# Kernel tuning notes

Measured on AMD Instinct MI355X. Metric: run time of the kernel, lower is better.

## Reference

```python
import jax, jax.numpy as jnp
import numpy as np

N = 100000
E = 1600000
F_IN = 64
H = 128
D_OUT = 1
G = 512  # number of graphs
EPS = 1e-5


def setup_inputs() -> dict:
    key = jax.random.key(0)
    ks = jax.random.split(key, 16)
    x = jax.random.normal(ks[0], (N, F_IN), dtype=jnp.float32)
    edge_index = jax.random.randint(ks[1], (2, E), 0, N, dtype=jnp.int64)
    batch = jnp.sort(jax.random.randint(ks[2], (N,), 0, G, dtype=jnp.int64))
    def lin(k, fin, fout):
        s = 1.0 / np.sqrt(fin)
        k1, k2 = jax.random.split(k)
        return (jax.random.uniform(k1, (fin, fout), jnp.float32, -s, s),
                jax.random.uniform(k2, (fout,), jnp.float32, -s, s))
    fc1_w, fc1_b = lin(ks[3], F_IN, H)
    gc1_w, gc1_b = lin(ks[4], H, H)
    gc2_w, gc2_b = lin(ks[5], H, H)
    fc2_w, fc2_b = lin(ks[6], H, D_OUT)
    gn1_g = jnp.ones((H,), jnp.float32); gn1_b = jnp.zeros((H,), jnp.float32)
    gn2_g = jnp.ones((H,), jnp.float32); gn2_b = jnp.zeros((H,), jnp.float32)
    return dict(x=x, edge_index=edge_index, batch=batch,
                fc1_w=fc1_w, fc1_b=fc1_b, gc1_w=gc1_w, gc1_b=gc1_b,
                gn1_g=gn1_g, gn1_b=gn1_b, gc2_w=gc2_w, gc2_b=gc2_b,
                gn2_g=gn2_g, gn2_b=gn2_b, fc2_w=fc2_w, fc2_b=fc2_b)


def gcn_conv(x, src, dst, deg_inv_sqrt, w, b):
    # x: [N,H]; symmetric-normalized aggregation with self-loops already in src/dst
    h = x @ w  # [N, H_out]
    norm = deg_inv_sqrt[src] * deg_inv_sqrt[dst]  # [E+N]
    msgs = h[src] * norm[:, None]
    out = jax.ops.segment_sum(msgs, dst, num_segments=N)
    return out + b


def graph_layernorm(x, batch, gamma, beta, counts):
    # PyG LayerNorm mode='graph': normalize over all nodes+channels per graph
    denom = jnp.maximum(counts * x.shape[1], 1.0)  # [G]
    mean = jax.ops.segment_sum(x.sum(-1), batch, num_segments=G) / denom
    xc = x - mean[batch][:, None]
    var = jax.ops.segment_sum((xc * xc).sum(-1), batch, num_segments=G) / denom
    inv = jax.lax.rsqrt(var + EPS)
    return xc * inv[batch][:, None] * gamma + beta


def reference(x, edge_index, batch, fc1_w, fc1_b, gc1_w, gc1_b, gn1_g, gn1_b,
              gc2_w, gc2_b, gn2_g, gn2_b, fc2_w, fc2_b):
    loops = jnp.arange(N, dtype=edge_index.dtype)
    src = jnp.concatenate([edge_index[0], loops])
    dst = jnp.concatenate([edge_index[1], loops])
    deg = jax.ops.segment_sum(jnp.ones_like(dst, dtype=x.dtype), dst, num_segments=N)
    deg_inv_sqrt = jnp.where(deg > 0, jax.lax.rsqrt(jnp.maximum(deg, 1.0)), 0.0)
    counts = jax.ops.segment_sum(jnp.ones_like(batch, dtype=x.dtype), batch, num_segments=G)

    hx = x @ fc1_w + fc1_b
    h = jax.nn.relu(graph_layernorm(gcn_conv(hx, src, dst, deg_inv_sqrt, gc1_w, gc1_b), batch, gn1_g, gn1_b, counts))
    h = jax.nn.relu(graph_layernorm(gcn_conv(h, src, dst, deg_inv_sqrt, gc2_w, gc2_b), batch, gn2_g, gn2_b, counts))
    pooled = jax.ops.segment_sum(h, batch, num_segments=G) / jnp.maximum(counts, 1.0)[:, None]
    return pooled @ fc2_w + fc2_b  # [G, D_OUT]
```

## Files before the change

### kernel.cpp

```cpp
#include <hip/hip_runtime.h>

#define NN 100000
#define EE 1600000
#define FIN 64
#define HH 128
#define GG 512
#define EPSV 1e-5f

__global__ void initk(int* deg, int* cursor, int* counts,
                      float* gsum1, float* gsq1, float* gsum2, float* gsq2,
                      float* pooled) {
  int i = blockIdx.x * 256 + threadIdx.x;
  if (i < NN) { deg[i] = 1; cursor[i] = 0; }
  if (i < GG) { counts[i] = 0; gsum1[i] = 0.f; gsq1[i] = 0.f; gsum2[i] = 0.f; gsq2[i] = 0.f; }
  if (i < GG * HH) pooled[i] = 0.f;
}

__global__ void countk(const int* __restrict__ ei, const int* __restrict__ batch,
                       int* deg, int* counts) {
  int i = blockIdx.x * 256 + threadIdx.x;
  if (i < EE) atomicAdd(&deg[ei[EE + i]], 1);
  if (i < NN) atomicAdd(&counts[batch[i]], 1);
}

__global__ void disk(const int* __restrict__ deg, float* __restrict__ dis) {
  int i = blockIdx.x * 256 + threadIdx.x;
  if (i < NN) dis[i] = rsqrtf((float)deg[i]);
}

#define SCHUNK 1024
__global__ void scan1(const int* __restrict__ deg, int* __restrict__ bsum) {
  __shared__ int red[256];
  int b = blockIdx.x, t = threadIdx.x;
  int base = b * SCHUNK + t * 4;
  int s = 0;
#pragma unroll
  for (int i = 0; i < 4; i++) { int idx = base + i; if (idx < NN) s += deg[idx] - 1; }
  red[t] = s; __syncthreads();
  for (int o = 128; o > 0; o >>= 1) { if (t < o) red[t] += red[t + o]; __syncthreads(); }
  if (t == 0) bsum[b] = red[0];
}

__global__ void scan2(const int* __restrict__ bsum, int* __restrict__ boff,
                      int* __restrict__ rowptr, int nblk) {
  if (threadIdx.x == 0 && blockIdx.x == 0) {
    int run = 0;
    for (int i = 0; i < nblk; i++) { boff[i] = run; run += bsum[i]; }
    rowptr[NN] = run;
  }
}

__global__ void scan3(const int* __restrict__ deg, const int* __restrict__ boff,
                      int* __restrict__ rowptr) {
  __shared__ int sc[2][256];
  int b = blockIdx.x, t = threadIdx.x;
  int base = b * SCHUNK + t * 4;
  int v[4]; int s = 0;
#pragma unroll
  for (int i = 0; i < 4; i++) {
    int idx = base + i;
    v[i] = (idx < NN) ? (deg[idx] - 1) : 0;
    s += v[i];
  }
  int pp = 0;
  sc[0][t] = s; __syncthreads();
  for (int o = 1; o < 256; o <<= 1) {
    int val = sc[pp][t];
    if (t >= o) val += sc[pp][t - o];
    sc[pp ^ 1][t] = val; __syncthreads();
    pp ^= 1;
  }
  int excl = sc[pp][t] - s;
  int p = boff[b] + excl;
#pragma unroll
  for (int i = 0; i < 4; i++) {
    int idx = base + i;
    if (idx < NN) rowptr[idx] = p;
    p += v[i];
  }
}

__global__ void scatterk(const int* __restrict__ ei, int* cursor,
                         const int* __restrict__ rowptr, int* __restrict__ colsrc) {
  int e = blockIdx.x * 256 + threadIdx.x;
  if (e >= EE) return;
  int d = ei[EE + e];
  int pos = rowptr[d] + atomicAdd(&cursor[d], 1);
  colsrc[pos] = ei[e];
}

__global__ void prepw(const float* __restrict__ fc1w, const float* __restrict__ fc1b,
                      const float* __restrict__ gc1w,
                      float* __restrict__ Wp, float* __restrict__ c1) {
  int k = blockIdx.x, t = threadIdx.x;
  if (k < 64) {
    float s = 0.f;
    for (int j = 0; j < 128; j++) s = fmaf(fc1w[k * 128 + j], gc1w[j * 128 + t], s);
    Wp[k * 128 + t] = s;
  } else {
    float s = 0.f;
    for (int j = 0; j < 128; j++) s = fmaf(fc1b[j], gc1w[j * 128 + t], s);
    c1[t] = s;
  }
}

__global__ __launch_bounds__(256, 8)
void aggx(const float* __restrict__ X, const int* __restrict__ colsrc,
          const int* __restrict__ rowptr, const float* __restrict__ dis,
          float* __restrict__ Y, float* __restrict__ rowsum) {
  int wid = threadIdx.x >> 6;
  int n = blockIdx.x * 4 + wid;
  int lane = threadIdx.x & 63;
  int slot = lane >> 4, q = lane & 15;
  float di = dis[n];
  int rp0 = rowptr[n];
  int m = rowptr[n + 1] - rp0 + 1;
  float4 acc = make_float4(0.f, 0.f, 0.f, 0.f);
  float wsum = 0.f;
  int s[4];
#pragma unroll
  for (int j = 0; j < 4; j++) {
    int idx = 4 * j + slot;
    s[j] = (idx >= m - 1) ? n : colsrc[rp0 + idx];
  }
  int p = 0;
  for (; p + 15 < m; p += 16) {
    int sn[4];
#pragma unroll
    for (int j = 0; j < 4; j++) {
      int idx = p + 16 + 4 * j + slot;
      sn[j] = (idx >= m - 1) ? n : colsrc[rp0 + idx];
    }
    float w[4]; float4 h[4];
#pragma unroll
    for (int j = 0; j < 4; j++) {
      w[j] = dis[s[j]] * di;
      h[j] = *reinterpret_cast<const float4*>(&X[(size_t)s[j] * FIN + q * 4]);
    }
#pragma unroll
    for (int j = 0; j < 4; j++) {
      acc.x = fmaf(h[j].x, w[j], acc.x);
      acc.y = fmaf(h[j].y, w[j], acc.y);
      acc.z = fmaf(h[j].z, w[j], acc.z);
      acc.w = fmaf(h[j].w, w[j], acc.w);
      wsum += w[j];
    }
#pragma unroll
    for (int j = 0; j < 4; j++) s[j] = sn[j];
  }
  for (; p < m; p += 4) {
    int idx = p + slot;
    if (idx < m) {
      int sv = (idx == m - 1) ? n : colsrc[rp0 + idx];
      float w = dis[sv] * di;
      float4 h = *reinterpret_cast<const float4*>(&X[(size_t)sv * FIN + q * 4]);
      acc.x = fmaf(h.x, w, acc.x);
      acc.y = fmaf(h.y, w, acc.y);
      acc.z = fmaf(h.z, w, acc.z);
      acc.w = fmaf(h.w, w, acc.w);
      wsum += w;
    }
  }
  acc.x += __shfl_xor(acc.x, 16); acc.y += __shfl_xor(acc.y, 16);
  acc.z += __shfl_xor(acc.z, 16); acc.w += __shfl_xor(acc.w, 16);
  wsum  += __shfl_xor(wsum, 16);
  acc.x += __shfl_xor(acc.x, 32); acc.y += __shfl_xor(acc.y, 32);
  acc.z += __shfl_xor(acc.z, 32); acc.w += __shfl_xor(acc.w, 32);
  wsum  += __shfl_xor(wsum, 32);
  if (slot == 0) {
    *reinterpret_cast<float4*>(&Y[(size_t)n * FIN + q * 4]) = acc;
  }
  if (lane == 0) rowsum[n] = wsum;
}

__global__ void gemmA(const float* __restrict__ Y, const float* __restrict__ Wp,
                      const float* __restrict__ c1, const float* __restrict__ gc1b,
                      const float* __restrict__ rowsum, const int* __restrict__ batch,
                      float* __restrict__ A, float* __restrict__ gsum, float* __restrict__ gsq) {
  __shared__ float ys[8 * 64];
  __shared__ float l1[8][2], l2[8][2];
  int n0 = blockIdx.x * 8, t = threadIdx.x;
  reinterpret_cast<float4*>(ys)[t] =
      reinterpret_cast<const float4*>(Y + (size_t)n0 * 64)[t];
  __syncthreads();
  float cv = c1[t], bv = gc1b[t];
  float acc[8];
#pragma unroll
  for (int n = 0; n < 8; n++) acc[n] = bv;
#pragma unroll 4
  for (int k = 0; k < 64; k++) {
    float wv = Wp[k * 128 + t];
#pragma unroll
    for (int n = 0; n < 8; n++) acc[n] = fmaf(ys[n * 64 + k], wv, acc[n]);
  }
#pragma unroll
  for (int n = 0; n < 8; n++) {
    acc[n] = fmaf(rowsum[n0 + n], cv, acc[n]);
    A[(size_t)(n0 + n) * 128 + t] = acc[n];
  }
  int wid = t >> 6, lane = t & 63;
#pragma unroll
  for (int n = 0; n < 8; n++) {
    float s1v = acc[n], s2v = acc[n] * acc[n];
    for (int o = 32; o > 0; o >>= 1) {
      s1v += __shfl_down(s1v, o);
      s2v += __shfl_down(s2v, o);
    }
    if (lane == 0) { l1[n][wid] = s1v; l2[n][wid] = s2v; }
  }
  __syncthreads();
  if (t < 8) {
    int b = batch[n0 + t];
    atomicAdd(&gsum[b], l1[t][0] + l1[t][1]);
    atomicAdd(&gsq[b], l2[t][0] + l2[t][1]);
  }
}

template <bool LN>
__global__ void gemm128(const float* __restrict__ X, const float* __restrict__ W,
                        float* __restrict__ Y,
                        const int* __restrict__ batch,
                        const float* __restrict__ mean, const float* __restrict__ inv,
                        const float* __restrict__ gamma, const float* __restrict__ beta) {
  __shared__ float xs[8 * 128];
  int n0 = blockIdx.x * 8, t = threadIdx.x;
  const float* xb = X + (size_t)n0 * 128;
  if (LN) {
#pragma unroll
    for (int j = 0; j < 8; j++) {
      int node = n0 + j;
      int bb = batch[node];
      float v = xb[j * 128 + t];
      v = (v - mean[bb]) * inv[bb] * gamma[t] + beta[t];
      xs[j * 128 + t] = fmaxf(v, 0.f);
    }
  } else {
    for (int i = t; i < 1024; i += 128) xs[i] = xb[i];
  }
  __syncthreads();
  float acc[8];
#pragma unroll
  for (int n = 0; n < 8; n++) acc[n] = 0.f;
#pragma unroll 4
  for (int k = 0; k < 128; k++) {
    float wv = W[k * 128 + t];
#pragma unroll
    for (int n = 0; n < 8; n++) acc[n] = fmaf(xs[n * 128 + k], wv, acc[n]);
  }
#pragma unroll
  for (int n = 0; n < 8; n++) Y[(size_t)(n0 + n) * 128 + t] = acc[n];
}

__global__ __launch_bounds__(256, 8)
void aggk(const float* __restrict__ Hin, const int* __restrict__ colsrc,
          const int* __restrict__ rowptr, const float* __restrict__ dis,
          const float* __restrict__ bias, const int* __restrict__ batch,
          float* __restrict__ Yout, float* __restrict__ gsum, float* __restrict__ gsq) {
  int wid = threadIdx.x >> 6;
  int n = blockIdx.x * 4 + wid;
  int lane = threadIdx.x & 63;
  int half = lane >> 5, q = lane & 31;
  float di = dis[n];
  int rp0 = rowptr[n];
  int m = rowptr[n + 1] - rp0 + 1;
  float4 acc = make_float4(0.f, 0.f, 0.f, 0.f);
  int s[4];
#pragma unroll
  for (int j = 0; j < 4; j++) {
    int idx = 2 * j + half;
    s[j] = (idx >= m - 1) ? n : colsrc[rp0 + idx];
  }
  int p = 0;
  for (; p + 7 < m; p += 8) {
    int sn[4];
#pragma unroll
    for (int j = 0; j < 4; j++) {
      int idx = p + 8 + 2 * j + half;
      sn[j] = (idx >= m - 1) ? n : colsrc[rp0 + idx];
    }
    float w[4]; float4 h[4];
#pragma unroll
    for (int j = 0; j < 4; j++) {
      w[j] = dis[s[j]] * di;
      h[j] = *reinterpret_cast<const float4*>(&Hin[(size_t)s[j] * HH + q * 4]);
    }
#pragma unroll
    for (int j = 0; j < 4; j++) {
      acc.x = fmaf(h[j].x, w[j], acc.x);
      acc.y = fmaf(h[j].y, w[j], acc.y);
      acc.z = fmaf(h[j].z, w[j], acc.z);
      acc.w = fmaf(h[j].w, w[j], acc.w);
    }
#pragma unroll
    for (int j = 0; j < 4; j++) s[j] = sn[j];
  }
  for (; p < m; p += 2) {
    int idx = p + half;
    if (idx < m) {
      int sv = (idx == m - 1) ? n : colsrc[rp0 + idx];
      float w = dis[sv] * di;
      float4 h = *reinterpret_cast<const float4*>(&Hin[(size_t)sv * HH + q * 4]);
      acc.x = fmaf(h.x, w, acc.x);
      acc.y = fmaf(h.y, w, acc.y);
      acc.z = fmaf(h.z, w, acc.z);
      acc.w = fmaf(h.w, w, acc.w);
    }
  }
  acc.x += __shfl_xor(acc.x, 32);
  acc.y += __shfl_xor(acc.y, 32);
  acc.z += __shfl_xor(acc.z, 32);
  acc.w += __shfl_xor(acc.w, 32);
  float4 bv = *reinterpret_cast<const float4*>(&bias[q * 4]);
  acc.x += bv.x; acc.y += bv.y; acc.z += bv.z; acc.w += bv.w;
  if (half == 0) {
    *reinterpret_cast<float4*>(&Yout[(size_t)n * HH + q * 4]) = acc;
  }
  float s1 = acc.x + acc.y + acc.z + acc.w;
  float s2 = acc.x * acc.x + acc.y * acc.y + acc.z * acc.z + acc.w * acc.w;
  for (int o = 16; o > 0; o >>= 1) {
    s1 += __shfl_down(s1, o);
    s2 += __shfl_down(s2, o);
  }
  if (lane == 0) {
    int b = batch[n];
    atomicAdd(&gsum[b], s1);
    atomicAdd(&gsq[b], s2);
  }
}

__global__ void lnfinal(const float* __restrict__ gsum, const float* __restrict__ gsq,
                        const int* __restrict__ counts,
                        float* __restrict__ mean, float* __restrict__ inv) {
  int g = blockIdx.x * 256 + threadIdx.x;
  if (g >= GG) return;
  float denom = fmaxf((float)counts[g] * (float)HH, 1.f);
  float m = gsum[g] / denom;
  float v = gsq[g] / denom - m * m;
  mean[g] = m;
  inv[g] = rsqrtf(fmaxf(v, 0.f) + EPSV);
}

__global__ void poolk(const float* __restrict__ A, const int* __restrict__ batch,
                      const float* __restrict__ mean, const float* __restrict__ inv,
                      const float* __restrict__ gamma, const float* __restrict__ beta,
                      float* __restrict__ pooled) {
  int idx = blockIdx.x * 256 + threadIdx.x;
  if (idx >= NN * HH) return;
  int n = idx >> 7, ch = idx & 127;
  int b = batch[n];
  float v = (A[idx] - mean[b]) * inv[b] * gamma[ch] + beta[ch];
  v = fmaxf(v, 0.f);
  atomicAdd(&pooled[b * 128 + ch], v);
}

__global__ void finalk(const float* __restrict__ pooled, const int* __restrict__ counts,
                       const float* __restrict__ w, const float* __restrict__ b,
                       float* __restrict__ out) {
  int g = blockIdx.x, t = threadIdx.x;
  float cnt = fmaxf((float)counts[g], 1.f);
  float v = pooled[g * 128 + t] / cnt * w[t];
  for (int o = 32; o > 0; o >>= 1) v += __shfl_down(v, o);
  __shared__ float l[2];
  if ((t & 63) == 0) l[t >> 6] = v;
  __syncthreads();
  if (t == 0) out[g] = l[0] + l[1] + b[0];
}

extern "C" void kernel_launch(void* const* d_in, const int* in_sizes, int n_in,
                              void* d_out, int out_size, void* d_ws, size_t ws_size,
                              hipStream_t stream) {
  const float* x = (const float*)d_in[0];
  const int* ei = (const int*)d_in[1];
  const int* batch = (const int*)d_in[2];
  const float* fc1_w = (const float*)d_in[3];
  const float* fc1_b = (const float*)d_in[4];
  const float* gc1_w = (const float*)d_in[5];
  const float* gc1_b = (const float*)d_in[6];
  const float* gn1_g = (const float*)d_in[7];
  const float* gn1_b = (const float*)d_in[8];
  const float* gc2_w = (const float*)d_in[9];
  const float* gc2_b = (const float*)d_in[10];
  const float* gn2_g = (const float*)d_in[11];
  const float* gn2_b = (const float*)d_in[12];
  const float* fc2_w = (const float*)d_in[13];
  const float* fc2_b = (const float*)d_in[14];
  float* out = (float*)d_out;

  char* p = (char*)d_ws;
  auto alloc = [&](size_t bytes) { void* r = (void*)p; p += ((bytes + 255) / 256) * 256; return r; };
  float* A = (float*)alloc((size_t)NN * HH * 4);
  float* B = (float*)alloc((size_t)NN * HH * 4);
  float* Yx = B;
  int* colsrc = (int*)alloc((size_t)EE * 4);
  int* rowptr = (int*)alloc((size_t)(NN + 1) * 4);
  int* deg = (int*)alloc((size_t)NN * 4);
  int* cursor = (int*)alloc((size_t)NN * 4);
  float* dis = (float*)alloc((size_t)NN * 4);
  float* rowsum = (float*)alloc((size_t)NN * 4);
  int* counts = (int*)alloc((size_t)GG * 4);
  float* gsum1 = (float*)alloc((size_t)GG * 4);
  float* gsq1 = (float*)alloc((size_t)GG * 4);
  float* gsum2 = (float*)alloc((size_t)GG * 4);
  float* gsq2 = (float*)alloc((size_t)GG * 4);
  float* mean1 = (float*)alloc((size_t)GG * 4);
  float* inv1 = (float*)alloc((size_t)GG * 4);
  float* mean2 = (float*)alloc((size_t)GG * 4);
  float* inv2 = (float*)alloc((size_t)GG * 4);
  float* pooled = (float*)alloc((size_t)GG * HH * 4);
  float* Wp = (float*)alloc((size_t)64 * 128 * 4);
  float* c1 = (float*)alloc((size_t)128 * 4);
  int* bsum = (int*)alloc(1024);
  int* boff = (int*)alloc(1024);

  int nblk = (NN + SCHUNK - 1) / SCHUNK;

  initk<<<(NN + 255) / 256, 256, 0, stream>>>(deg, cursor, counts, gsum1, gsq1, gsum2, gsq2, pooled);
  countk<<<(EE + 255) / 256, 256, 0, stream>>>(ei, batch, deg, counts);
  disk<<<(NN + 255) / 256, 256, 0, stream>>>(deg, dis);
  scan1<<<nblk, 256, 0, stream>>>(deg, bsum);
  scan2<<<1, 64, 0, stream>>>(bsum, boff, rowptr, nblk);
  scan3<<<nblk, 256, 0, stream>>>(deg, boff, rowptr);
  scatterk<<<(EE + 255) / 256, 256, 0, stream>>>(ei, cursor, rowptr, colsrc);
  prepw<<<65, 128, 0, stream>>>(fc1_w, fc1_b, gc1_w, Wp, c1);

  aggx<<<NN / 4, 256, 0, stream>>>(x, colsrc, rowptr, dis, Yx, rowsum);
  gemmA<<<NN / 8, 128, 0, stream>>>(Yx, Wp, c1, gc1_b, rowsum, batch, A, gsum1, gsq1);
  lnfinal<<<(GG + 255) / 256, 256, 0, stream>>>(gsum1, gsq1, counts, mean1, inv1);
  gemm128<true><<<NN / 8, 128, 0, stream>>>(A, gc2_w, B, batch, mean1, inv1, gn1_g, gn1_b);
  aggk<<<NN / 4, 256, 0, stream>>>(B, colsrc, rowptr, dis, gc2_b, batch, A, gsum2, gsq2);
  lnfinal<<<(GG + 255) / 256, 256, 0, stream>>>(gsum2, gsq2, counts, mean2, inv2);
  poolk<<<(NN * HH + 255) / 256, 256, 0, stream>>>(A, batch, mean2, inv2, gn2_g, gn2_b, pooled);
  finalk<<<GG, 128, 0, stream>>>(pooled, counts, fc2_w, fc2_b, out);
}
```

Measured before the change: 1.040 ms.

## Store gathered node features in bf16 for both aggregation passes

Converts the input features x to bf16 in a new pre-pass and makes the second-layer GEMM write its output as bf16. Both gather-based aggregation kernels now read bf16 rows, so each gathered row moves half the bytes, and they accumulate in fp32. The per-lane layout is reworked so each lane handles 8 channels, which changes edge parallelism and the shuffle reductions. This adds an extra conversion kernel and lowers the precision of the aggregated features, which could affect accuracy tolerances.

```diff
diff --git a/kernel.cpp b/kernel.cpp
--- a/kernel.cpp
+++ b/kernel.cpp
@@ -6,6 +6,12 @@
 #define HH 128
 #define GG 512
 #define EPSV 1e-5f
+
+__device__ __forceinline__ unsigned short f2bf(float f) {
+  unsigned int u = __float_as_uint(f);
+  u = (u + 0x7FFFu + ((u >> 16) & 1u)) >> 16;
+  return (unsigned short)u;
+}
 
 __global__ void initk(int* deg, int* cursor, int* counts,
                       float* gsum1, float* gsq1, float* gsum2, float* gsq2,
@@ -14,6 +20,15 @@
   if (i < NN) { deg[i] = 1; cursor[i] = 0; }
   if (i < GG) { counts[i] = 0; gsum1[i] = 0.f; gsq1[i] = 0.f; gsum2[i] = 0.f; gsq2[i] = 0.f; }
   if (i < GG * HH) pooled[i] = 0.f;
+}
+
+__global__ void convx(const float* __restrict__ x, unsigned short* __restrict__ xb) {
+  int i = blockIdx.x * 256 + threadIdx.x;
+  if (i >= NN * FIN / 4) return;
+  float4 v = reinterpret_cast<const float4*>(x)[i];
+  ushort4 o;
+  o.x = f2bf(v.x); o.y = f2bf(v.y); o.z = f2bf(v.z); o.w = f2bf(v.w);
+  reinterpret_cast<ushort4*>(xb)[i] = o;
 }
 
 __global__ void countk(const int* __restrict__ ei, const int* __restrict__ batch,
@@ -105,70 +120,76 @@
 }
 
 __global__ __launch_bounds__(256, 8)
-void aggx(const float* __restrict__ X, const int* __restrict__ colsrc,
+void aggx(const unsigned short* __restrict__ X, const int* __restrict__ colsrc,
           const int* __restrict__ rowptr, const float* __restrict__ dis,
           float* __restrict__ Y, float* __restrict__ rowsum) {
   int wid = threadIdx.x >> 6;
   int n = blockIdx.x * 4 + wid;
   int lane = threadIdx.x & 63;
-  int slot = lane >> 4, q = lane & 15;
+  int slot = lane >> 3, q = lane & 7;
   float di = dis[n];
   int rp0 = rowptr[n];
   int m = rowptr[n + 1] - rp0 + 1;
-  float4 acc = make_float4(0.f, 0.f, 0.f, 0.f);
+  float acc[8];
+#pragma unroll
+  for (int k = 0; k < 8; k++) acc[k] = 0.f;
   float wsum = 0.f;
-  int s[4];
-#pragma unroll
-  for (int j = 0; j < 4; j++) {
-    int idx = 4 * j + slot;
-    s[j] = (idx >= m - 1) ? n : colsrc[rp0 + idx];
-  }
   int p = 0;
   for (; p + 15 < m; p += 16) {
-    int sn[4];
-#pragma unroll
-    for (int j = 0; j < 4; j++) {
-      int idx = p + 16 + 4 * j + slot;
-      sn[j] = (idx >= m - 1) ? n : colsrc[rp0 + idx];
-    }
-    float w[4]; float4 h[4];
-#pragma unroll
-    for (int j = 0; j < 4; j++) {
+    int s[2]; float w[2]; uint4 h[2];
+#pragma unroll
+    for (int j = 0; j < 2; j++) {
+      int idx = p + 8 * j + slot;
+      s[j] = (idx == m - 1) ? n : colsrc[rp0 + idx];
+    }
+#pragma unroll
+    for (int j = 0; j < 2; j++) {
       w[j] = dis[s[j]] * di;
-      h[j] = *reinterpret_cast<const float4*>(&X[(size_t)s[j] * FIN + q * 4]);
-    }
-#pragma unroll
-    for (int j = 0; j < 4; j++) {
-      acc.x = fmaf(h[j].x, w[j], acc.x);
-      acc.y = fmaf(h[j].y, w[j], acc.y);
-      acc.z = fmaf(h[j].z, w[j], acc.z);
-      acc.w = fmaf(h[j].w, w[j], acc.w);
+      h[j] = reinterpret_cast<const uint4*>(X + (size_t)s[j] * FIN)[q];
+    }
+#pragma unroll
+    for (int j = 0; j < 2; j++) {
+      unsigned int u;
+      u = h[j].x; acc[0] = fmaf(__uint_as_float(u << 16), w[j], acc[0]);
+                  acc[1] = fmaf(__uint_as_float(u & 0xFFFF0000u), w[j], acc[1]);
+      u = h[j].y; acc[2] = fmaf(__uint_as_float(u << 16), w[j], acc[2]);
+                  acc[3] = fmaf(__uint_as_float(u & 0xFFFF0000u), w[j], acc[3]);
+      u = h[j].z; acc[4] = fmaf(__uint_as_float(u << 16), w[j], acc[4]);
+                  acc[5] = fmaf(__uint_as_float(u & 0xFFFF0000u), w[j], acc[5]);
+      u = h[j].w; acc[6] = fmaf(__uint_as_float(u << 16), w[j], acc[6]);
+                  acc[7] = fmaf(__uint_as_float(u & 0xFFFF0000u), w[j], acc[7]);
       wsum += w[j];
     }
-#pragma unroll
-    for (int j = 0; j < 4; j++) s[j] = sn[j];
-  }
-  for (; p < m; p += 4) {
+  }
+  for (; p < m; p += 8) {
     int idx = p + slot;
     if (idx < m) {
       int sv = (idx == m - 1) ? n : colsrc[rp0 + idx];
       float w = dis[sv] * di;
-      float4 h = *reinterpret_cast<const float4*>(&X[(size_t)sv * FIN + q * 4]);
-      acc.x = fmaf(h.x, w, acc.x);
-      acc.y = fmaf(h.y, w, acc.y);
-      acc.z = fmaf(h.z, w, acc.z);
-      acc.w = fmaf(h.w, w, acc.w);
+      uint4 h = reinterpret_cast<const uint4*>(X + (size_t)sv * FIN)[q];
+      unsigned int u;
+      u = h.x; acc[0] = fmaf(__uint_as_float(u << 16), w, acc[0]);
+               acc[1] = fmaf(__uint_as_float(u & 0xFFFF0000u), w, acc[1]);
+      u = h.y; acc[2] = fmaf(__uint_as_float(u << 16), w, acc[2]);
+               acc[3] = fmaf(__uint_as_float(u & 0xFFFF0000u), w, acc[3]);
+      u = h.z; acc[4] = fmaf(__uint_as_float(u << 16), w, acc[4]);
+               acc[5] = fmaf(__uint_as_float(u & 0xFFFF0000u), w, acc[5]);
+      u = h.w; acc[6] = fmaf(__uint_as_float(u << 16), w, acc[6]);
+               acc[7] = fmaf(__uint_as_float(u & 0xFFFF0000u), w, acc[7]);
       wsum += w;
     }
   }
-  acc.x += __shfl_xor(acc.x, 16); acc.y += __shfl_xor(acc.y, 16);
-  acc.z += __shfl_xor(acc.z, 16); acc.w += __shfl_xor(acc.w, 16);
-  wsum  += __shfl_xor(wsum, 16);
-  acc.x += __shfl_xor(acc.x, 32); acc.y += __shfl_xor(acc.y, 32);
-  acc.z += __shfl_xor(acc.z, 32); acc.w += __shfl_xor(acc.w, 32);
-  wsum  += __shfl_xor(wsum, 32);
+#pragma unroll
+  for (int o = 8; o <= 32; o <<= 1) {
+#pragma unroll
+    for (int k = 0; k < 8; k++) acc[k] += __shfl_xor(acc[k], o);
+    wsum += __shfl_xor(wsum, o);
+  }
   if (slot == 0) {
-    *reinterpret_cast<float4*>(&Y[(size_t)n * FIN + q * 4]) = acc;
+    float4 a = make_float4(acc[0], acc[1], acc[2], acc[3]);
+    float4 b = make_float4(acc[4], acc[5], acc[6], acc[7]);
+    reinterpret_cast<float4*>(&Y[(size_t)n * FIN + q * 8])[0] = a;
+    reinterpret_cast<float4*>(&Y[(size_t)n * FIN + q * 8])[1] = b;
   }
   if (lane == 0) rowsum[n] = wsum;
 }
@@ -216,26 +237,21 @@
   }
 }
 
-template <bool LN>
 __global__ void gemm128(const float* __restrict__ X, const float* __restrict__ W,
-                        float* __restrict__ Y,
+                        unsigned short* __restrict__ Yb,
                         const int* __restrict__ batch,
                         const float* __restrict__ mean, const float* __restrict__ inv,
                         const float* __restrict__ gamma, const float* __restrict__ beta) {
   __shared__ float xs[8 * 128];
   int n0 = blockIdx.x * 8, t = threadIdx.x;
   const float* xb = X + (size_t)n0 * 128;
-  if (LN) {
-#pragma unroll
-    for (int j = 0; j < 8; j++) {
-      int node = n0 + j;
-      int bb = batch[node];
-      float v = xb[j * 128 + t];
-      v = (v - mean[bb]) * inv[bb] * gamma[t] + beta[t];
-      xs[j * 128 + t] = fmaxf(v, 0.f);
-    }
-  } else {
-    for (int i = t; i < 1024; i += 128) xs[i] = xb[i];
+#pragma unroll
+  for (int j = 0; j < 8; j++) {
+    int node = n0 + j;
+    int bb = batch[node];
+    float v = xb[j * 128 + t];
+    v = (v - mean[bb]) * inv[bb] * gamma[t] + beta[t];
+    xs[j * 128 + t] = fmaxf(v, 0.f);
   }
   __syncthreads();
   float acc[8];
@@ -248,76 +264,86 @@
     for (int n = 0; n < 8; n++) acc[n] = fmaf(xs[n * 128 + k], wv, acc[n]);
   }
 #pragma unroll
-  for (int n = 0; n < 8; n++) Y[(size_t)(n0 + n) * 128 + t] = acc[n];
+  for (int n = 0; n < 8; n++) Yb[(size_t)(n0 + n) * 128 + t] = f2bf(acc[n]);
 }
 
 __global__ __launch_bounds__(256, 8)
-void aggk(const float* __restrict__ Hin, const int* __restrict__ colsrc,
+void aggk(const unsigned short* __restrict__ Hin, const int* __restrict__ colsrc,
           const int* __restrict__ rowptr, const float* __restrict__ dis,
           const float* __restrict__ bias, const int* __restrict__ batch,
           float* __restrict__ Yout, float* __restrict__ gsum, float* __restrict__ gsq) {
   int wid = threadIdx.x >> 6;
   int n = blockIdx.x * 4 + wid;
   int lane = threadIdx.x & 63;
-  int half = lane >> 5, q = lane & 31;
+  int slot = lane >> 4, q = lane & 15;
   float di = dis[n];
   int rp0 = rowptr[n];
   int m = rowptr[n + 1] - rp0 + 1;
-  float4 acc = make_float4(0.f, 0.f, 0.f, 0.f);
-  int s[4];
-#pragma unroll
-  for (int j = 0; j < 4; j++) {
-    int idx = 2 * j + half;
-    s[j] = (idx >= m - 1) ? n : colsrc[rp0 + idx];
-  }
+  float acc[8];
+#pragma unroll
+  for (int k = 0; k < 8; k++) acc[k] = 0.f;
   int p = 0;
-  for (; p + 7 < m; p += 8) {
-    int sn[4];
+  for (; p + 15 < m; p += 16) {
+    int s[4]; float w[4]; uint4 h[4];
 #pragma unroll
     for (int j = 0; j < 4; j++) {
-      int idx = p + 8 + 2 * j + half;
-      sn[j] = (idx >= m - 1) ? n : colsrc[rp0 + idx];
-    }
-    float w[4]; float4 h[4];
+      int idx = p + 4 * j + slot;
+      s[j] = (idx == m - 1) ? n : colsrc[rp0 + idx];
+    }
 #pragma unroll
     for (int j = 0; j < 4; j++) {
       w[j] = dis[s[j]] * di;
-      h[j] = *reinterpret_cast<const float4*>(&Hin[(size_t)s[j] * HH + q * 4]);
+      h[j] = reinterpret_cast<const uint4*>(Hin + (size_t)s[j] * HH)[q];
     }
 #pragma unroll
     for (int j = 0; j < 4; j++) {
-      acc.x = fmaf(h[j].x, w[j], acc.x);
-      acc.y = fmaf(h[j].y, w[j], acc.y);
-      acc.z = fmaf(h[j].z, w[j], acc.z);
-      acc.w = fmaf(h[j].w, w[j], acc.w);
-    }
-#pragma unroll
-    for (int j = 0; j < 4; j++) s[j] = sn[j];
-  }
-  for (; p < m; p += 2) {
-    int idx = p + half;
+      unsigned int u;
+      u = h[j].x; acc[0] = fmaf(__uint_as_float(u << 16), w[j], acc[0]);
+                  acc[1] = fmaf(__uint_as_float(u & 0xFFFF0000u), w[j], acc[1]);
+      u = h[j].y; acc[2] = fmaf(__uint_as_float(u << 16), w[j], acc[2]);
+                  acc[3] = fmaf(__uint_as_float(u & 0xFFFF0000u), w[j], acc[3]);
+      u = h[j].z; acc[4] = fmaf(__uint_as_float(u << 16), w[j], acc[4]);
+                  acc[5] = fmaf(__uint_as_float(u & 0xFFFF0000u), w[j], acc[5]);
+      u = h[j].w; acc[6] = fmaf(__uint_as_float(u << 16), w[j], acc[6]);
+                  acc[7] = fmaf(__uint_as_float(u & 0xFFFF0000u), w[j], acc[7]);
+    }
+  }
+  for (; p < m; p += 4) {
+    int idx = p + slot;
     if (idx < m) {
       int sv = (idx == m - 1) ? n : colsrc[rp0 + idx];
       float w = dis[sv] * di;
-      float4 h = *reinterpret_cast<const float4*>(&Hin[(size_t)sv * HH + q * 4]);
-      acc.x = fmaf(h.x, w, acc.x);
-      acc.y = fmaf(h.y, w, acc.y);
-      acc.z = fmaf(h.z, w, acc.z);
-      acc.w = fmaf(h.w, w, acc.w);
-    }
-  }
-  acc.x += __shfl_xor(acc.x, 32);
-  acc.y += __shfl_xor(acc.y, 32);
-  acc.z += __shfl_xor(acc.z, 32);
-  acc.w += __shfl_xor(acc.w, 32);
-  float4 bv = *reinterpret_cast<const float4*>(&bias[q * 4]);
-  acc.x += bv.x; acc.y += bv.y; acc.z += bv.z; acc.w += bv.w;
-  if (half == 0) {
-    *reinterpret_cast<float4*>(&Yout[(size_t)n * HH + q * 4]) = acc;
-  }
-  float s1 = acc.x + acc.y + acc.z + acc.w;
-  float s2 = acc.x * acc.x + acc.y * acc.y + acc.z * acc.z + acc.w * acc.w;
-  for (int o = 16; o > 0; o >>= 1) {
+      uint4 h = reinterpret_cast<const uint4*>(Hin + (size_t)sv * HH)[q];
+      unsigned int u;
+      u = h.x; acc[0] = fmaf(__uint_as_float(u << 16), w, acc[0]);
+               acc[1] = fmaf(__uint_as_float(u & 0xFFFF0000u), w, acc[1]);
+      u = h.y; acc[2] = fmaf(__uint_as_float(u << 16), w, acc[2]);
+               acc[3] = fmaf(__uint_as_float(u & 0xFFFF0000u), w, acc[3]);
+      u = h.z; acc[4] = fmaf(__uint_as_float(u << 16), w, acc[4]);
+               acc[5] = fmaf(__uint_as_float(u & 0xFFFF0000u), w, acc[5]);
+      u = h.w; acc[6] = fmaf(__uint_as_float(u << 16), w, acc[6]);
+               acc[7] = fmaf(__uint_as_float(u & 0xFFFF0000u), w, acc[7]);
+    }
+  }
+#pragma unroll
+  for (int o = 16; o <= 32; o <<= 1) {
+#pragma unroll
+    for (int k = 0; k < 8; k++) acc[k] += __shfl_xor(acc[k], o);
+  }
+  float4 b0 = reinterpret_cast<const float4*>(&bias[q * 8])[0];
+  float4 b1 = reinterpret_cast<const float4*>(&bias[q * 8])[1];
+  acc[0] += b0.x; acc[1] += b0.y; acc[2] += b0.z; acc[3] += b0.w;
+  acc[4] += b1.x; acc[5] += b1.y; acc[6] += b1.z; acc[7] += b1.w;
+  if (slot == 0) {
+    float4 a = make_float4(acc[0], acc[1], acc[2], acc[3]);
+    float4 b = make_float4(acc[4], acc[5], acc[6], acc[7]);
+    reinterpret_cast<float4*>(&Yout[(size_t)n * HH + q * 8])[0] = a;
+    reinterpret_cast<float4*>(&Yout[(size_t)n * HH + q * 8])[1] = b;
+  }
+  float s1 = acc[0] + acc[1] + acc[2] + acc[3] + acc[4] + acc[5] + acc[6] + acc[7];
+  float s2 = acc[0] * acc[0] + acc[1] * acc[1] + acc[2] * acc[2] + acc[3] * acc[3] +
+             acc[4] * acc[4] + acc[5] * acc[5] + acc[6] * acc[6] + acc[7] * acc[7];
+  for (int o = 8; o > 0; o >>= 1) {
     s1 += __shfl_down(s1, o);
     s2 += __shfl_down(s2, o);
   }
@@ -391,6 +417,8 @@
   float* A = (float*)alloc((size_t)NN * HH * 4);
   float* B = (float*)alloc((size_t)NN * HH * 4);
   float* Yx = B;
+  unsigned short* Bb = (unsigned short*)B;
+  unsigned short* xb = (unsigned short*)(A + (size_t)NN * 96);
   int* colsrc = (int*)alloc((size_t)EE * 4);
   int* rowptr = (int*)alloc((size_t)(NN + 1) * 4);
   int* deg = (int*)alloc((size_t)NN * 4);
@@ -415,6 +443,7 @@
   int nblk = (NN + SCHUNK - 1) / SCHUNK;
 
   initk<<<(NN + 255) / 256, 256, 0, stream>>>(deg, cursor, counts, gsum1, gsq1, gsum2, gsq2, pooled);
+  convx<<<(NN * FIN / 4 + 255) / 256, 256, 0, stream>>>(x, xb);
   countk<<<(EE + 255) / 256, 256, 0, stream>>>(ei, batch, deg, counts);
   disk<<<(NN + 255) / 256, 256, 0, stream>>>(deg, dis);
   scan1<<<nblk, 256, 0, stream>>>(deg, bsum);
@@ -423,11 +452,11 @@
   scatterk<<<(EE + 255) / 256, 256, 0, stream>>>(ei, cursor, rowptr, colsrc);
   prepw<<<65, 128, 0, stream>>>(fc1_w, fc1_b, gc1_w, Wp, c1);
 
-  aggx<<<NN / 4, 256, 0, stream>>>(x, colsrc, rowptr, dis, Yx, rowsum);
+  aggx<<<NN / 4, 256, 0, stream>>>(xb, colsrc, rowptr, dis, Yx, rowsum);
   gemmA<<<NN / 8, 128, 0, stream>>>(Yx, Wp, c1, gc1_b, rowsum, batch, A, gsum1, gsq1);
   lnfinal<<<(GG + 255) / 256, 256, 0, stream>>>(gsum1, gsq1, counts, mean1, inv1);
-  gemm128<true><<<NN / 8, 128, 0, stream>>>(A, gc2_w, B, batch, mean1, inv1, gn1_g, gn1_b);
-  aggk<<<NN / 4, 256, 0, stream>>>(B, colsrc, rowptr, dis, gc2_b, batch, A, gsum2, gsq2);
+  gemm128<<<NN / 8, 128, 0, stream>>>(A, gc2_w, Bb, batch, mean1, inv1, gn1_g, gn1_b);
+  aggk<<<NN / 4, 256, 0, stream>>>(Bb, colsrc, rowptr, dis, gc2_b, batch, A, gsum2, gsq2);
   lnfinal<<<(GG + 255) / 256, 256, 0, stream>>>(gsum2, gsq2, counts, mean2, inv2);
   poolk<<<(NN * HH + 255) / 256, 256, 0, stream>>>(A, batch, mean2, inv2, gn2_g, gn2_b, pooled);
   finalk<<<GG, 128, 0, stream>>>(pooled, counts, fc2_w, fc2_b, out);
```

Measured after the change: 946.2 us. -9.0%, faster.
